# Optimization experiments

Measured on AMD Instinct MI355X. Metric: run time of the kernel, lower is better.

## Reference

```python
import jax, jax.numpy as jnp
import numpy as np

N_NODES = 50000
N_EDGES = 800000
NFEAT, NHID, NCLASS = 128, 256, 64


def setup_inputs() -> dict:
    key = jax.random.key(0)
    ks = jax.random.split(key, 8)
    x = jax.random.normal(ks[0], (N_NODES, NFEAT), dtype=jnp.float32)
    edge_index = jax.random.randint(ks[1], (2, N_EDGES), 0, N_NODES, dtype=jnp.int64)
    s1 = 1.0 / np.sqrt(NFEAT)
    s2 = 1.0 / np.sqrt(NHID)
    W1_neigh = jax.random.normal(ks[2], (NFEAT, NHID), dtype=jnp.float32) * s1
    W1_root = jax.random.normal(ks[3], (NFEAT, NHID), dtype=jnp.float32) * s1
    b1 = jnp.zeros((NHID,), dtype=jnp.float32)
    W2_neigh = jax.random.normal(ks[4], (NHID, NCLASS), dtype=jnp.float32) * s2
    W2_root = jax.random.normal(ks[5], (NHID, NCLASS), dtype=jnp.float32) * s2
    b2 = jnp.zeros((NCLASS,), dtype=jnp.float32)
    return {"x": x, "edge_index": edge_index, "W1_neigh": W1_neigh,
            "W1_root": W1_root, "b1": b1, "W2_neigh": W2_neigh,
            "W2_root": W2_root, "b2": b2}


def _sage_conv(h, src, dst, n_nodes, W_neigh, W_root, b):
    # mean aggregation of source features into destination nodes
    msg = h[src]                                                   # [E, d]
    summed = jax.ops.segment_sum(msg, dst, num_segments=n_nodes)   # [N, d]
    cnt = jax.ops.segment_sum(jnp.ones((src.shape[0],), h.dtype), dst,
                              num_segments=n_nodes)                # [N]
    mean = summed / jnp.maximum(cnt, 1.0)[:, None]
    return mean @ W_neigh + h @ W_root + b


def reference(x, edge_index, W1_neigh, W1_root, b1, W2_neigh, W2_root, b2):
    src, dst = edge_index[0], edge_index[1]
    n = x.shape[0]
    h = jax.nn.relu(_sage_conv(x, src, dst, n, W1_neigh, W1_root, b1))
    # dropout is identity in eval mode
    out = _sage_conv(h, src, dst, n, W2_neigh, W2_root, b2)
    return out
```

## Files before the change

### kernel.cpp

```cpp
#include <hip/hip_runtime.h>

#define N_NODES 50000
#define N_EDGES 800000
#define NFEAT   128
#define NHID    256
#define NCLASS  64

#define NPASS 8
#define PASS_W ((N_NODES + NPASS - 1) / NPASS)
#define ELLCAP 64

#define NPAIR   (N_EDGES / 2)
#define ECHUNK2 ((NPAIR + 255) / 256)
#define FILL_B  (ECHUNK2 * NPASS)
#define CVTX_B  ((N_NODES * 32 + 255) / 256)
#define CVTW_B  (((65536 + 32768) + 255) / 256)

typedef unsigned short u16;
typedef unsigned int   u32;
typedef __attribute__((ext_vector_type(8))) u16   u16x8;
typedef __attribute__((ext_vector_type(8))) short s16x8;
typedef __attribute__((ext_vector_type(4))) float f32x4;

__device__ inline u16 f2bf(float f) {
    u32 u = __float_as_uint(f);
    u32 r = (u + 0x7FFFu + ((u >> 16) & 1u)) >> 16;
    return (u16)r;
}
__device__ inline float bflo(u32 v) { return __uint_as_float(v << 16); }
__device__ inline float bfhi(u32 v) { return __uint_as_float(v & 0xFFFF0000u); }

#define GLOAD_LDS16(g, l)                                                        \
    __builtin_amdgcn_global_load_lds(                                            \
        (const __attribute__((address_space(1))) u32*)(const void*)(g),          \
        (__attribute__((address_space(3))) u32*)(void*)(l), 16, 0, 0)

__global__ __launch_bounds__(256) void prep_fill_kernel(const float* __restrict__ x,
                                                        const int* __restrict__ ei,
                                                        const float* __restrict__ W1r,
                                                        const float* __restrict__ W1n,
                                                        const float* __restrict__ W2n,
                                                        const float* __restrict__ W2r,
                                                        u16* __restrict__ xa,
                                                        int* __restrict__ cnt,
                                                        u16* __restrict__ ell,
                                                        u16* __restrict__ W1t,
                                                        u16* __restrict__ W2t) {
    int b = blockIdx.x;
    if (b < FILL_B) {
        int p = b & (NPASS - 1);
        int i = (b >> 3) * 256 + threadIdx.x;
        if (i >= NPAIR) return;
        int2 d2 = reinterpret_cast<const int2*>(ei + N_EDGES)[i];
        u32 lo = (u32)(p * PASS_W);
        bool in0 = ((u32)d2.x - lo) < (u32)PASS_W;
        bool in1 = ((u32)d2.y - lo) < (u32)PASS_W;
        if (in0 | in1) {
            int2 s2 = reinterpret_cast<const int2*>(ei)[i];
            if (in0) {
                int pos = atomicAdd(&cnt[d2.x], 1);
                if (pos < ELLCAP) ell[(size_t)d2.x * ELLCAP + pos] = (u16)s2.x;
            }
            if (in1) {
                int pos = atomicAdd(&cnt[d2.y], 1);
                if (pos < ELLCAP) ell[(size_t)d2.y * ELLCAP + pos] = (u16)s2.y;
            }
        }
    } else if (b < FILL_B + CVTX_B) {
        int idx = (b - FILL_B) * 256 + threadIdx.x;
        if (idx >= N_NODES * 32) return;
        int r  = idx >> 5;
        int c4 = (idx & 31) * 4;
        float4 v = *reinterpret_cast<const float4*>(x + (size_t)r * NFEAT + c4);
        uint2 o;
        o.x = (u32)f2bf(v.x) | ((u32)f2bf(v.y) << 16);
        o.y = (u32)f2bf(v.z) | ((u32)f2bf(v.w) << 16);
        *reinterpret_cast<uint2*>(xa + (size_t)r * 256 + c4) = o;
    } else {
        int id = (b - FILL_B - CVTX_B) * 256 + threadIdx.x;
        if (id < 65536) {
            int k = id & 255, n = id >> 8;
            float v = (k < NFEAT) ? W1r[(size_t)k * NHID + n]
                                  : W1n[(size_t)(k - NFEAT) * NHID + n];
            W1t[(size_t)n * 256 + k] = f2bf(v);
        } else if (id < 65536 + 32768) {
            int j = id - 65536;
            int k = j & 255, n = j >> 8;
            float v = (n < NCLASS) ? W2n[(size_t)k * NCLASS + n]
                                   : W2r[(size_t)k * NCLASS + (n - NCLASS)];
            W2t[(size_t)n * 256 + k] = f2bf(v);
        }
    }
}

__global__ __launch_bounds__(256) void gather1_kernel(const int* __restrict__ cnt,
                                                      const u16* __restrict__ ell,
                                                      u16* __restrict__ xa) {
    int gtid = blockIdx.x * 256 + threadIdx.x;
    int node = gtid >> 6;
    if (node >= N_NODES) return;
    int lane = threadIdx.x & 63;
    const u32* xrow = reinterpret_cast<const u32*>(xa);
    const u16* idx = ell + (size_t)node * ELLCAP;
    int deg = cnt[node];
    if (deg > ELLCAP) deg = ELLCAP;
    float ax = 0.0f, ay = 0.0f;
    int j = 0;
    for (; j + 16 <= deg; j += 16) {
        int s[16]; u32 v[16];
        #pragma unroll
        for (int q = 0; q < 16; ++q) s[q] = idx[j + q];
        #pragma unroll
        for (int q = 0; q < 16; ++q) v[q] = xrow[(size_t)s[q] * 128 + lane];
        #pragma unroll
        for (int q = 0; q < 16; ++q) { ax += bflo(v[q]); ay += bfhi(v[q]); }
    }
    for (; j + 8 <= deg; j += 8) {
        int s[8]; u32 v[8];
        #pragma unroll
        for (int q = 0; q < 8; ++q) s[q] = idx[j + q];
        #pragma unroll
        for (int q = 0; q < 8; ++q) v[q] = xrow[(size_t)s[q] * 128 + lane];
        #pragma unroll
        for (int q = 0; q < 8; ++q) { ax += bflo(v[q]); ay += bfhi(v[q]); }
    }
    for (; j < deg; ++j) {
        u32 v = xrow[(size_t)idx[j] * 128 + lane];
        ax += bflo(v);
        ay += bfhi(v);
    }
    float invd = 1.0f / fmaxf((float)deg, 1.0f);
    u32 packed = (u32)f2bf(ax * invd) | ((u32)f2bf(ay * invd) << 16);
    reinterpret_cast<u32*>(xa + (size_t)node * 256 + 128)[lane] = packed;
}

__global__ __launch_bounds__(256) void gather2_kernel(const int* __restrict__ cnt,
                                                      const u16* __restrict__ ell,
                                                      const u16* __restrict__ t,
                                                      float* __restrict__ out) {
    int gtid = blockIdx.x * 256 + threadIdx.x;
    int wave = gtid >> 6;
    int lane = threadIdx.x & 63;
    int node = wave * 2 + (lane >> 5);
    int l    = lane & 31;
    if (node >= N_NODES) return;
    const u32* trow = reinterpret_cast<const u32*>(t);
    const u16* idx = ell + (size_t)node * ELLCAP;
    int deg = cnt[node];
    if (deg > ELLCAP) deg = ELLCAP;
    float ax = 0.0f, ay = 0.0f;
    int j = 0;
    for (; j + 16 <= deg; j += 16) {
        int s[16]; u32 v[16];
        #pragma unroll
        for (int q = 0; q < 16; ++q) s[q] = idx[j + q];
        #pragma unroll
        for (int q = 0; q < 16; ++q) v[q] = trow[(size_t)s[q] * 32 + l];
        #pragma unroll
        for (int q = 0; q < 16; ++q) { ax += bflo(v[q]); ay += bfhi(v[q]); }
    }
    for (; j + 8 <= deg; j += 8) {
        int s[8]; u32 v[8];
        #pragma unroll
        for (int q = 0; q < 8; ++q) s[q] = idx[j + q];
        #pragma unroll
        for (int q = 0; q < 8; ++q) v[q] = trow[(size_t)s[q] * 32 + l];
        #pragma unroll
        for (int q = 0; q < 8; ++q) { ax += bflo(v[q]); ay += bfhi(v[q]); }
    }
    for (; j < deg; ++j) {
        u32 v = trow[(size_t)idx[j] * 32 + l];
        ax += bflo(v); ay += bfhi(v);
    }
    float invd = 1.0f / fmaxf((float)deg, 1.0f);
    float* o = out + (size_t)node * NCLASS + l * 2;
    o[0] += ax * invd;
    o[1] += ay * invd;
}

__global__ __launch_bounds__(256) void gemm1_mfma(const u16* __restrict__ xa,
                                                  const u16* __restrict__ W1t,
                                                  const float* __restrict__ b1,
                                                  u16* __restrict__ h) {
    __shared__ u16 As[128 * 32];
    __shared__ u16 Bs[128 * 32];
    const int tid = threadIdx.x;
    const int r0 = blockIdx.x * 128;
    const int n0 = blockIdx.y * 128;
    const int wid = tid >> 6, ln = tid & 63;
    const int wm = (wid & 1) * 64, wn = (wid >> 1) * 64;
    const int lr = ln & 15;
    const int lq = ln >> 4;

    f32x4 acc[4][4] = {};

    for (int k0 = 0; k0 < 256; k0 += 32) {
        #pragma unroll
        for (int it = 0; it < 2; ++it) {
            int c   = it * 256 + tid;
            int row = c >> 2;
            int ko  = (c & 3) * 8;
            GLOAD_LDS16(xa  + (size_t)(r0 + row) * 256 + k0 + ko, As + c * 8);
            GLOAD_LDS16(W1t + (size_t)(n0 + row) * 256 + k0 + ko, Bs + c * 8);
        }
        __syncthreads();

        s16x8 af[4], bf[4];
        #pragma unroll
        for (int i = 0; i < 4; ++i)
            af[i] = *reinterpret_cast<const s16x8*>(As + (wm + i * 16 + lr) * 32 + lq * 8);
        #pragma unroll
        for (int j = 0; j < 4; ++j)
            bf[j] = *reinterpret_cast<const s16x8*>(Bs + (wn + j * 16 + lr) * 32 + lq * 8);
        #pragma unroll
        for (int i = 0; i < 4; ++i)
            #pragma unroll
            for (int j = 0; j < 4; ++j)
                acc[i][j] = __builtin_amdgcn_mfma_f32_16x16x32_bf16(af[i], bf[j], acc[i][j], 0, 0, 0);
        __syncthreads();
    }

    #pragma unroll
    for (int i = 0; i < 4; ++i) {
        #pragma unroll
        for (int j = 0; j < 4; ++j) {
            int col = n0 + wn + j * 16 + lr;
            float bias = b1[col];
            #pragma unroll
            for (int r = 0; r < 4; ++r) {
                int row = r0 + wm + i * 16 + lq * 4 + r;
                if (row < N_NODES)
                    h[(size_t)row * 256 + col] = f2bf(fmaxf(acc[i][j][r] + bias, 0.0f));
            }
        }
    }
}

__global__ __launch_bounds__(256) void gemm2_mfma(const u16* __restrict__ h,
                                                  const u16* __restrict__ W2t,
                                                  const float* __restrict__ b2,
                                                  u16* __restrict__ t,
                                                  float* __restrict__ out) {
    __shared__ u16 As[128 * 32];
    __shared__ u16 Bs[128 * 32];
    const int tid = threadIdx.x;
    const int r0 = blockIdx.x * 128;
    const int wid = tid >> 6, ln = tid & 63;
    const int wm = (wid & 1) * 64, wn = (wid >> 1) * 64;
    const int lr = ln & 15;
    const int lq = ln >> 4;

    f32x4 acc[4][4] = {};

    for (int k0 = 0; k0 < 256; k0 += 32) {
        #pragma unroll
        for (int it = 0; it < 2; ++it) {
            int c   = it * 256 + tid;
            int row = c >> 2;
            int ko  = (c & 3) * 8;
            GLOAD_LDS16(h   + (size_t)(r0 + row) * 256 + k0 + ko, As + c * 8);
            GLOAD_LDS16(W2t + (size_t)row * 256 + k0 + ko,        Bs + c * 8);
        }
        __syncthreads();

        s16x8 af[4], bf[4];
        #pragma unroll
        for (int i = 0; i < 4; ++i)
            af[i] = *reinterpret_cast<const s16x8*>(As + (wm + i * 16 + lr) * 32 + lq * 8);
        #pragma unroll
        for (int j = 0; j < 4; ++j)
            bf[j] = *reinterpret_cast<const s16x8*>(Bs + (wn + j * 16 + lr) * 32 + lq * 8);
        #pragma unroll
        for (int i = 0; i < 4; ++i)
            #pragma unroll
            for (int j = 0; j < 4; ++j)
                acc[i][j] = __builtin_amdgcn_mfma_f32_16x16x32_bf16(af[i], bf[j], acc[i][j], 0, 0, 0);
        __syncthreads();
    }

    #pragma unroll
    for (int i = 0; i < 4; ++i) {
        #pragma unroll
        for (int j = 0; j < 4; ++j) {
            int col = wn + j * 16 + lr;
            #pragma unroll
            for (int r = 0; r < 4; ++r) {
                int row = r0 + wm + i * 16 + lq * 4 + r;
                if (row >= N_NODES) continue;
                if (col < NCLASS) {
                    t[(size_t)row * NCLASS + col] = f2bf(acc[i][j][r]);
                } else {
                    int c = col - NCLASS;
                    out[(size_t)row * NCLASS + c] = acc[i][j][r] + b2[c];
                }
            }
        }
    }
}

extern "C" void kernel_launch(void* const* d_in, const int* in_sizes, int n_in,
                              void* d_out, int out_size, void* d_ws, size_t ws_size,
                              hipStream_t stream) {
    const float* x    = (const float*)d_in[0];
    const int*   ei   = (const int*)d_in[1];
    const float* W1n  = (const float*)d_in[2];
    const float* W1r  = (const float*)d_in[3];
    const float* b1   = (const float*)d_in[4];
    const float* W2n  = (const float*)d_in[5];
    const float* W2r  = (const float*)d_in[6];
    const float* b2   = (const float*)d_in[7];
    float* out = (float*)d_out;

    int* cnt = (int*)d_ws;
    u16* ell = (u16*)(cnt + 50048);
    u16* xa  = ell + (size_t)N_NODES * ELLCAP;
    u16* h   = xa + (size_t)N_NODES * 256;
    u16* t   = h  + (size_t)N_NODES * 256;
    u16* W1t = t  + (size_t)N_NODES * 64;
    u16* W2t = W1t + 65536;

    hipMemsetAsync(cnt, 0, 50048 * sizeof(int), stream);

    prep_fill_kernel<<<FILL_B + CVTX_B + CVTW_B, 256, 0, stream>>>(
        x, ei, W1r, W1n, W2n, W2r, xa, cnt, ell, W1t, W2t);

    gather1_kernel<<<(N_NODES * 64 + 255) / 256, 256, 0, stream>>>(cnt, ell, xa);
    gemm1_mfma<<<dim3((N_NODES + 127) / 128, 2), 256, 0, stream>>>(xa, W1t, b1, h);

    gemm2_mfma<<<(N_NODES + 127) / 128, 256, 0, stream>>>(h, W2t, b2, t, out);
    gather2_kernel<<<(N_NODES * 32 + 255) / 256, 256, 0, stream>>>(cnt, ell, t, out);
}
```

Before: 227.4 us.

## Fuse all stages into one persistent cooperative kernel with grid syncs

```diff
diff --git a/kernel.cpp b/kernel.cpp
--- a/kernel.cpp
+++ b/kernel.cpp
@@ -1,4 +1,7 @@
 #include <hip/hip_runtime.h>
+#include <hip/hip_cooperative_groups.h>
+
+namespace cg = cooperative_groups;
 
 #define N_NODES 50000
 #define N_EDGES 800000
@@ -15,6 +18,9 @@
 #define FILL_B  (ECHUNK2 * NPASS)
 #define CVTX_B  ((N_NODES * 32 + 255) / 256)
 #define CVTW_B  (((65536 + 32768) + 255) / 256)
+
+#define G1_TILES 782
+#define G2_TILES 391
 
 typedef unsigned short u16;
 typedef unsigned int   u32;
@@ -35,265 +41,263 @@
         (const __attribute__((address_space(1))) u32*)(const void*)(g),          \
         (__attribute__((address_space(3))) u32*)(void*)(l), 16, 0, 0)
 
-__global__ __launch_bounds__(256) void prep_fill_kernel(const float* __restrict__ x,
-                                                        const int* __restrict__ ei,
-                                                        const float* __restrict__ W1r,
-                                                        const float* __restrict__ W1n,
-                                                        const float* __restrict__ W2n,
-                                                        const float* __restrict__ W2r,
-                                                        u16* __restrict__ xa,
-                                                        int* __restrict__ cnt,
-                                                        u16* __restrict__ ell,
-                                                        u16* __restrict__ W1t,
-                                                        u16* __restrict__ W2t) {
-    int b = blockIdx.x;
-    if (b < FILL_B) {
-        int p = b & (NPASS - 1);
-        int i = (b >> 3) * 256 + threadIdx.x;
-        if (i >= NPAIR) return;
-        int2 d2 = reinterpret_cast<const int2*>(ei + N_EDGES)[i];
-        u32 lo = (u32)(p * PASS_W);
-        bool in0 = ((u32)d2.x - lo) < (u32)PASS_W;
-        bool in1 = ((u32)d2.y - lo) < (u32)PASS_W;
-        if (in0 | in1) {
-            int2 s2 = reinterpret_cast<const int2*>(ei)[i];
-            if (in0) {
-                int pos = atomicAdd(&cnt[d2.x], 1);
-                if (pos < ELLCAP) ell[(size_t)d2.x * ELLCAP + pos] = (u16)s2.x;
-            }
-            if (in1) {
-                int pos = atomicAdd(&cnt[d2.y], 1);
-                if (pos < ELLCAP) ell[(size_t)d2.y * ELLCAP + pos] = (u16)s2.y;
-            }
-        }
-    } else if (b < FILL_B + CVTX_B) {
-        int idx = (b - FILL_B) * 256 + threadIdx.x;
-        if (idx >= N_NODES * 32) return;
-        int r  = idx >> 5;
-        int c4 = (idx & 31) * 4;
-        float4 v = *reinterpret_cast<const float4*>(x + (size_t)r * NFEAT + c4);
-        uint2 o;
-        o.x = (u32)f2bf(v.x) | ((u32)f2bf(v.y) << 16);
-        o.y = (u32)f2bf(v.z) | ((u32)f2bf(v.w) << 16);
-        *reinterpret_cast<uint2*>(xa + (size_t)r * 256 + c4) = o;
-    } else {
-        int id = (b - FILL_B - CVTX_B) * 256 + threadIdx.x;
-        if (id < 65536) {
-            int k = id & 255, n = id >> 8;
-            float v = (k < NFEAT) ? W1r[(size_t)k * NHID + n]
-                                  : W1n[(size_t)(k - NFEAT) * NHID + n];
-            W1t[(size_t)n * 256 + k] = f2bf(v);
-        } else if (id < 65536 + 32768) {
-            int j = id - 65536;
-            int k = j & 255, n = j >> 8;
-            float v = (n < NCLASS) ? W2n[(size_t)k * NCLASS + n]
-                                   : W2r[(size_t)k * NCLASS + (n - NCLASS)];
-            W2t[(size_t)n * 256 + k] = f2bf(v);
-        }
-    }
-}
-
-__global__ __launch_bounds__(256) void gather1_kernel(const int* __restrict__ cnt,
-                                                      const u16* __restrict__ ell,
-                                                      u16* __restrict__ xa) {
-    int gtid = blockIdx.x * 256 + threadIdx.x;
-    int node = gtid >> 6;
-    if (node >= N_NODES) return;
-    int lane = threadIdx.x & 63;
-    const u32* xrow = reinterpret_cast<const u32*>(xa);
-    const u16* idx = ell + (size_t)node * ELLCAP;
-    int deg = cnt[node];
-    if (deg > ELLCAP) deg = ELLCAP;
-    float ax = 0.0f, ay = 0.0f;
-    int j = 0;
-    for (; j + 16 <= deg; j += 16) {
-        int s[16]; u32 v[16];
-        #pragma unroll
-        for (int q = 0; q < 16; ++q) s[q] = idx[j + q];
-        #pragma unroll
-        for (int q = 0; q < 16; ++q) v[q] = xrow[(size_t)s[q] * 128 + lane];
-        #pragma unroll
-        for (int q = 0; q < 16; ++q) { ax += bflo(v[q]); ay += bfhi(v[q]); }
-    }
-    for (; j + 8 <= deg; j += 8) {
-        int s[8]; u32 v[8];
-        #pragma unroll
-        for (int q = 0; q < 8; ++q) s[q] = idx[j + q];
-        #pragma unroll
-        for (int q = 0; q < 8; ++q) v[q] = xrow[(size_t)s[q] * 128 + lane];
-        #pragma unroll
-        for (int q = 0; q < 8; ++q) { ax += bflo(v[q]); ay += bfhi(v[q]); }
-    }
-    for (; j < deg; ++j) {
-        u32 v = xrow[(size_t)idx[j] * 128 + lane];
-        ax += bflo(v);
-        ay += bfhi(v);
-    }
-    float invd = 1.0f / fmaxf((float)deg, 1.0f);
-    u32 packed = (u32)f2bf(ax * invd) | ((u32)f2bf(ay * invd) << 16);
-    reinterpret_cast<u32*>(xa + (size_t)node * 256 + 128)[lane] = packed;
-}
-
-__global__ __launch_bounds__(256) void gather2_kernel(const int* __restrict__ cnt,
-                                                      const u16* __restrict__ ell,
-                                                      const u16* __restrict__ t,
-                                                      float* __restrict__ out) {
-    int gtid = blockIdx.x * 256 + threadIdx.x;
-    int wave = gtid >> 6;
-    int lane = threadIdx.x & 63;
-    int node = wave * 2 + (lane >> 5);
-    int l    = lane & 31;
-    if (node >= N_NODES) return;
-    const u32* trow = reinterpret_cast<const u32*>(t);
-    const u16* idx = ell + (size_t)node * ELLCAP;
-    int deg = cnt[node];
-    if (deg > ELLCAP) deg = ELLCAP;
-    float ax = 0.0f, ay = 0.0f;
-    int j = 0;
-    for (; j + 16 <= deg; j += 16) {
-        int s[16]; u32 v[16];
-        #pragma unroll
-        for (int q = 0; q < 16; ++q) s[q] = idx[j + q];
-        #pragma unroll
-        for (int q = 0; q < 16; ++q) v[q] = trow[(size_t)s[q] * 32 + l];
-        #pragma unroll
-        for (int q = 0; q < 16; ++q) { ax += bflo(v[q]); ay += bfhi(v[q]); }
-    }
-    for (; j + 8 <= deg; j += 8) {
-        int s[8]; u32 v[8];
-        #pragma unroll
-        for (int q = 0; q < 8; ++q) s[q] = idx[j + q];
-        #pragma unroll
-        for (int q = 0; q < 8; ++q) v[q] = trow[(size_t)s[q] * 32 + l];
-        #pragma unroll
-        for (int q = 0; q < 8; ++q) { ax += bflo(v[q]); ay += bfhi(v[q]); }
-    }
-    for (; j < deg; ++j) {
-        u32 v = trow[(size_t)idx[j] * 32 + l];
-        ax += bflo(v); ay += bfhi(v);
-    }
-    float invd = 1.0f / fmaxf((float)deg, 1.0f);
-    float* o = out + (size_t)node * NCLASS + l * 2;
-    o[0] += ax * invd;
-    o[1] += ay * invd;
-}
-
-__global__ __launch_bounds__(256) void gemm1_mfma(const u16* __restrict__ xa,
-                                                  const u16* __restrict__ W1t,
-                                                  const float* __restrict__ b1,
-                                                  u16* __restrict__ h) {
+__global__ __launch_bounds__(256) void uber_kernel(
+    const float* __restrict__ x,   const int* __restrict__ ei,
+    const float* __restrict__ W1r, const float* __restrict__ W1n,
+    const float* __restrict__ W2n, const float* __restrict__ W2r,
+    const float* __restrict__ b1,  const float* __restrict__ b2,
+    int* __restrict__ cnt, u16* __restrict__ ell,
+    u16* __restrict__ xa,  u16* __restrict__ h, u16* __restrict__ t,
+    u16* __restrict__ W1t, u16* __restrict__ W2t,
+    float* __restrict__ out)
+{
+    cg::grid_group grid = cg::this_grid();
+    const int tid = threadIdx.x;
+    const int nb  = gridDim.x;
+
     __shared__ u16 As[128 * 32];
     __shared__ u16 Bs[128 * 32];
-    const int tid = threadIdx.x;
-    const int r0 = blockIdx.x * 128;
-    const int n0 = blockIdx.y * 128;
-    const int wid = tid >> 6, ln = tid & 63;
-    const int wm = (wid & 1) * 64, wn = (wid >> 1) * 64;
-    const int lr = ln & 15;
-    const int lq = ln >> 4;
-
-    f32x4 acc[4][4] = {};
-
-    for (int k0 = 0; k0 < 256; k0 += 32) {
-        #pragma unroll
-        for (int it = 0; it < 2; ++it) {
-            int c   = it * 256 + tid;
-            int row = c >> 2;
-            int ko  = (c & 3) * 8;
-            GLOAD_LDS16(xa  + (size_t)(r0 + row) * 256 + k0 + ko, As + c * 8);
-            GLOAD_LDS16(W1t + (size_t)(n0 + row) * 256 + k0 + ko, Bs + c * 8);
-        }
-        __syncthreads();
-
-        s16x8 af[4], bf[4];
-        #pragma unroll
-        for (int i = 0; i < 4; ++i)
-            af[i] = *reinterpret_cast<const s16x8*>(As + (wm + i * 16 + lr) * 32 + lq * 8);
-        #pragma unroll
-        for (int j = 0; j < 4; ++j)
-            bf[j] = *reinterpret_cast<const s16x8*>(Bs + (wn + j * 16 + lr) * 32 + lq * 8);
-        #pragma unroll
-        for (int i = 0; i < 4; ++i)
+
+    for (int i = blockIdx.x * 256 + tid; i < 50048; i += nb * 256) cnt[i] = 0;
+    grid.sync();
+
+    for (int b = blockIdx.x; b < FILL_B + CVTX_B + CVTW_B; b += nb) {
+        if (b < FILL_B) {
+            int p = b & (NPASS - 1);
+            int i = (b >> 3) * 256 + tid;
+            if (i < NPAIR) {
+                int2 d2 = reinterpret_cast<const int2*>(ei + N_EDGES)[i];
+                u32 lo = (u32)(p * PASS_W);
+                bool in0 = ((u32)d2.x - lo) < (u32)PASS_W;
+                bool in1 = ((u32)d2.y - lo) < (u32)PASS_W;
+                if (in0 | in1) {
+                    int2 s2 = reinterpret_cast<const int2*>(ei)[i];
+                    if (in0) {
+                        int pos = atomicAdd(&cnt[d2.x], 1);
+                        if (pos < ELLCAP) ell[(size_t)d2.x * ELLCAP + pos] = (u16)s2.x;
+                    }
+                    if (in1) {
+                        int pos = atomicAdd(&cnt[d2.y], 1);
+                        if (pos < ELLCAP) ell[(size_t)d2.y * ELLCAP + pos] = (u16)s2.y;
+                    }
+                }
+            }
+        } else if (b < FILL_B + CVTX_B) {
+            int idx = (b - FILL_B) * 256 + tid;
+            if (idx < N_NODES * 32) {
+                int r  = idx >> 5;
+                int c4 = (idx & 31) * 4;
+                float4 v = *reinterpret_cast<const float4*>(x + (size_t)r * NFEAT + c4);
+                uint2 o;
+                o.x = (u32)f2bf(v.x) | ((u32)f2bf(v.y) << 16);
+                o.y = (u32)f2bf(v.z) | ((u32)f2bf(v.w) << 16);
+                *reinterpret_cast<uint2*>(xa + (size_t)r * 256 + c4) = o;
+            }
+        } else {
+            int id = (b - FILL_B - CVTX_B) * 256 + tid;
+            if (id < 65536) {
+                int k = id & 255, n = id >> 8;
+                float v = (k < NFEAT) ? W1r[(size_t)k * NHID + n]
+                                      : W1n[(size_t)(k - NFEAT) * NHID + n];
+                W1t[(size_t)n * 256 + k] = f2bf(v);
+            } else if (id < 65536 + 32768) {
+                int j = id - 65536;
+                int k = j & 255, n = j >> 8;
+                float v = (n < NCLASS) ? W2n[(size_t)k * NCLASS + n]
+                                       : W2r[(size_t)k * NCLASS + (n - NCLASS)];
+                W2t[(size_t)n * 256 + k] = f2bf(v);
+            }
+        }
+    }
+    grid.sync();
+
+    {
+        const u32* xrow = reinterpret_cast<const u32*>(xa);
+        int lane   = tid & 63;
+        int gwave  = (blockIdx.x * 256 + tid) >> 6;
+        int nwaves = (nb * 256) >> 6;
+        for (int node = gwave; node < N_NODES; node += nwaves) {
+            const u16* idx = ell + (size_t)node * ELLCAP;
+            int deg = cnt[node];
+            if (deg > ELLCAP) deg = ELLCAP;
+            float ax = 0.0f, ay = 0.0f;
+            int j = 0;
+            for (; j + 16 <= deg; j += 16) {
+                int s[16]; u32 v[16];
+                #pragma unroll
+                for (int q = 0; q < 16; ++q) s[q] = idx[j + q];
+                #pragma unroll
+                for (int q = 0; q < 16; ++q) v[q] = xrow[(size_t)s[q] * 128 + lane];
+                #pragma unroll
+                for (int q = 0; q < 16; ++q) { ax += bflo(v[q]); ay += bfhi(v[q]); }
+            }
+            for (; j + 8 <= deg; j += 8) {
+                int s[8]; u32 v[8];
+                #pragma unroll
+                for (int q = 0; q < 8; ++q) s[q] = idx[j + q];
+                #pragma unroll
+                for (int q = 0; q < 8; ++q) v[q] = xrow[(size_t)s[q] * 128 + lane];
+                #pragma unroll
+                for (int q = 0; q < 8; ++q) { ax += bflo(v[q]); ay += bfhi(v[q]); }
+            }
+            for (; j < deg; ++j) {
+                u32 v = xrow[(size_t)idx[j] * 128 + lane];
+                ax += bflo(v);
+                ay += bfhi(v);
+            }
+            float invd = 1.0f / fmaxf((float)deg, 1.0f);
+            u32 packed = (u32)f2bf(ax * invd) | ((u32)f2bf(ay * invd) << 16);
+            reinterpret_cast<u32*>(xa + (size_t)node * 256 + 128)[lane] = packed;
+        }
+    }
+    grid.sync();
+
+    {
+        const int wid = tid >> 6, ln = tid & 63;
+        const int wm = (wid & 1) * 64, wn = (wid >> 1) * 64;
+        const int lr = ln & 15;
+        const int lq = ln >> 4;
+        for (int vb = blockIdx.x; vb < G1_TILES; vb += nb) {
+            int by = (vb >= 391) ? 1 : 0;
+            int bx = vb - 391 * by;
+            int r0 = bx * 128, n0 = by * 128;
+
+            f32x4 acc[4][4] = {};
+            for (int k0 = 0; k0 < 256; k0 += 32) {
+                #pragma unroll
+                for (int it = 0; it < 2; ++it) {
+                    int c   = it * 256 + tid;
+                    int row = c >> 2;
+                    int ko  = (c & 3) * 8;
+                    GLOAD_LDS16(xa  + (size_t)(r0 + row) * 256 + k0 + ko, As + c * 8);
+                    GLOAD_LDS16(W1t + (size_t)(n0 + row) * 256 + k0 + ko, Bs + c * 8);
+                }
+                __syncthreads();
+                s16x8 af[4], bf[4];
+                #pragma unroll
+                for (int i = 0; i < 4; ++i)
+                    af[i] = *reinterpret_cast<const s16x8*>(As + (wm + i * 16 + lr) * 32 + lq * 8);
+                #pragma unroll
+                for (int j = 0; j < 4; ++j)
+                    bf[j] = *reinterpret_cast<const s16x8*>(Bs + (wn + j * 16 + lr) * 32 + lq * 8);
+                #pragma unroll
+                for (int i = 0; i < 4; ++i)
+                    #pragma unroll
+                    for (int j = 0; j < 4; ++j)
+                        acc[i][j] = __builtin_amdgcn_mfma_f32_16x16x32_bf16(af[i], bf[j], acc[i][j], 0, 0, 0);
+                __syncthreads();
+            }
             #pragma unroll
-            for (int j = 0; j < 4; ++j)
-                acc[i][j] = __builtin_amdgcn_mfma_f32_16x16x32_bf16(af[i], bf[j], acc[i][j], 0, 0, 0);
-        __syncthreads();
-    }
-
-    #pragma unroll
-    for (int i = 0; i < 4; ++i) {
-        #pragma unroll
-        for (int j = 0; j < 4; ++j) {
-            int col = n0 + wn + j * 16 + lr;
-            float bias = b1[col];
+            for (int i = 0; i < 4; ++i) {
+                #pragma unroll
+                for (int j = 0; j < 4; ++j) {
+                    int col = n0 + wn + j * 16 + lr;
+                    float bias = b1[col];
+                    #pragma unroll
+                    for (int r = 0; r < 4; ++r) {
+                        int row = r0 + wm + i * 16 + lq * 4 + r;
+                        if (row < N_NODES)
+                            h[(size_t)row * 256 + col] = f2bf(fmaxf(acc[i][j][r] + bias, 0.0f));
+                    }
+                }
+            }
+        }
+    }
+    grid.sync();
+
+    {
+        const int wid = tid >> 6, ln = tid & 63;
+        const int wm = (wid & 1) * 64, wn = (wid >> 1) * 64;
+        const int lr = ln & 15;
+        const int lq = ln >> 4;
+        for (int vb = blockIdx.x; vb < G2_TILES; vb += nb) {
+            int r0 = vb * 128;
+            f32x4 acc[4][4] = {};
+            for (int k0 = 0; k0 < 256; k0 += 32) {
+                #pragma unroll
+                for (int it = 0; it < 2; ++it) {
+                    int c   = it * 256 + tid;
+                    int row = c >> 2;
+                    int ko  = (c & 3) * 8;
+                    GLOAD_LDS16(h   + (size_t)(r0 + row) * 256 + k0 + ko, As + c * 8);
+                    GLOAD_LDS16(W2t + (size_t)row * 256 + k0 + ko,        Bs + c * 8);
+                }
+                __syncthreads();
+                s16x8 af[4], bf[4];
+                #pragma unroll
+                for (int i = 0; i < 4; ++i)
+                    af[i] = *reinterpret_cast<const s16x8*>(As + (wm + i * 16 + lr) * 32 + lq * 8);
+                #pragma unroll
+                for (int j = 0; j < 4; ++j)
+                    bf[j] = *reinterpret_cast<const s16x8*>(Bs + (wn + j * 16 + lr) * 32 + lq * 8);
+                #pragma unroll
+                for (int i = 0; i < 4; ++i)
+                    #pragma unroll
+                    for (int j = 0; j < 4; ++j)
+                        acc[i][j] = __builtin_amdgcn_mfma_f32_16x16x32_bf16(af[i], bf[j], acc[i][j], 0, 0, 0);
+                __syncthreads();
+            }
             #pragma unroll
-            for (int r = 0; r < 4; ++r) {
-                int row = r0 + wm + i * 16 + lq * 4 + r;
-                if (row < N_NODES)
-                    h[(size_t)row * 256 + col] = f2bf(fmaxf(acc[i][j][r] + bias, 0.0f));
-            }
-        }
-    }
-}
-
-__global__ __launch_bounds__(256) void gemm2_mfma(const u16* __restrict__ h,
-                                                  const u16* __restrict__ W2t,
-                                                  const float* __restrict__ b2,
-                                                  u16* __restrict__ t,
-                                                  float* __restrict__ out) {
-    __shared__ u16 As[128 * 32];
-    __shared__ u16 Bs[128 * 32];
-    const int tid = threadIdx.x;
-    const int r0 = blockIdx.x * 128;
-    const int wid = tid >> 6, ln = tid & 63;
-    const int wm = (wid & 1) * 64, wn = (wid >> 1) * 64;
-    const int lr = ln & 15;
-    const int lq = ln >> 4;
-
-    f32x4 acc[4][4] = {};
-
-    for (int k0 = 0; k0 < 256; k0 += 32) {
-        #pragma unroll
-        for (int it = 0; it < 2; ++it) {
-            int c   = it * 256 + tid;
-            int row = c >> 2;
-            int ko  = (c & 3) * 8;
-            GLOAD_LDS16(h   + (size_t)(r0 + row) * 256 + k0 + ko, As + c * 8);
-            GLOAD_LDS16(W2t + (size_t)row * 256 + k0 + ko,        Bs + c * 8);
-        }
-        __syncthreads();
-
-        s16x8 af[4], bf[4];
-        #pragma unroll
-        for (int i = 0; i < 4; ++i)
-            af[i] = *reinterpret_cast<const s16x8*>(As + (wm + i * 16 + lr) * 32 + lq * 8);
-        #pragma unroll
-        for (int j = 0; j < 4; ++j)
-            bf[j] = *reinterpret_cast<const s16x8*>(Bs + (wn + j * 16 + lr) * 32 + lq * 8);
-        #pragma unroll
-        for (int i = 0; i < 4; ++i)
-            #pragma unroll
-            for (int j = 0; j < 4; ++j)
-                acc[i][j] = __builtin_amdgcn_mfma_f32_16x16x32_bf16(af[i], bf[j], acc[i][j], 0, 0, 0);
-        __syncthreads();
-    }
-
-    #pragma unroll
-    for (int i = 0; i < 4; ++i) {
-        #pragma unroll
-        for (int j = 0; j < 4; ++j) {
-            int col = wn + j * 16 + lr;
-            #pragma unroll
-            for (int r = 0; r < 4; ++r) {
-                int row = r0 + wm + i * 16 + lq * 4 + r;
-                if (row >= N_NODES) continue;
-                if (col < NCLASS) {
-                    t[(size_t)row * NCLASS + col] = f2bf(acc[i][j][r]);
-                } else {
-                    int c = col - NCLASS;
-                    out[(size_t)row * NCLASS + c] = acc[i][j][r] + b2[c];
-                }
-            }
+            for (int i = 0; i < 4; ++i) {
+                #pragma unroll
+                for (int j = 0; j < 4; ++j) {
+                    int col = wn + j * 16 + lr;
+                    #pragma unroll
+                    for (int r = 0; r < 4; ++r) {
+                        int row = r0 + wm + i * 16 + lq * 4 + r;
+                        if (row >= N_NODES) continue;
+                        if (col < NCLASS) {
+                            t[(size_t)row * NCLASS + col] = f2bf(acc[i][j][r]);
+                        } else {
+                            int c = col - NCLASS;
+                            out[(size_t)row * NCLASS + c] = acc[i][j][r] + b2[c];
+                        }
+                    }
+                }
+            }
+        }
+    }
+    grid.sync();
+
+    {
+        const u32* trow = reinterpret_cast<const u32*>(t);
+        int lane   = tid & 63;
+        int gwave  = (blockIdx.x * 256 + tid) >> 6;
+        int nwaves = (nb * 256) >> 6;
+        int l    = lane & 31;
+        for (int w = gwave; w < N_NODES / 2; w += nwaves) {
+            int node = w * 2 + (lane >> 5);
+            const u16* idx = ell + (size_t)node * ELLCAP;
+            int deg = cnt[node];
+            if (deg > ELLCAP) deg = ELLCAP;
+            float ax = 0.0f, ay = 0.0f;
+            int j = 0;
+            for (; j + 16 <= deg; j += 16) {
+                int s[16]; u32 v[16];
+                #pragma unroll
+                for (int q = 0; q < 16; ++q) s[q] = idx[j + q];
+                #pragma unroll
+                for (int q = 0; q < 16; ++q) v[q] = trow[(size_t)s[q] * 32 + l];
+                #pragma unroll
+                for (int q = 0; q < 16; ++q) { ax += bflo(v[q]); ay += bfhi(v[q]); }
+            }
+            for (; j + 8 <= deg; j += 8) {
+                int s[8]; u32 v[8];
+                #pragma unroll
+                for (int q = 0; q < 8; ++q) s[q] = idx[j + q];
+                #pragma unroll
+                for (int q = 0; q < 8; ++q) v[q] = trow[(size_t)s[q] * 32 + l];
+                #pragma unroll
+                for (int q = 0; q < 8; ++q) { ax += bflo(v[q]); ay += bfhi(v[q]); }
+            }
+            for (; j < deg; ++j) {
+                u32 v = trow[(size_t)idx[j] * 32 + l];
+                ax += bflo(v); ay += bfhi(v);
+            }
+            float invd = 1.0f / fmaxf((float)deg, 1.0f);
+            float* o = out + (size_t)node * NCLASS + l * 2;
+            o[0] += ax * invd;
+            o[1] += ay * invd;
         }
     }
 }
@@ -319,14 +323,16 @@
     u16* W1t = t  + (size_t)N_NODES * 64;
     u16* W2t = W1t + 65536;
 
-    hipMemsetAsync(cnt, 0, 50048 * sizeof(int), stream);
-
-    prep_fill_kernel<<<FILL_B + CVTX_B + CVTW_B, 256, 0, stream>>>(
-        x, ei, W1r, W1n, W2n, W2r, xa, cnt, ell, W1t, W2t);
-
-    gather1_kernel<<<(N_NODES * 64 + 255) / 256, 256, 0, stream>>>(cnt, ell, xa);
-    gemm1_mfma<<<dim3((N_NODES + 127) / 128, 2), 256, 0, stream>>>(xa, W1t, b1, h);
-
-    gemm2_mfma<<<(N_NODES + 127) / 128, 256, 0, stream>>>(h, W2t, b2, t, out);
-    gather2_kernel<<<(N_NODES * 32 + 255) / 256, 256, 0, stream>>>(cnt, ell, t, out);
+    int occ = 0;
+    hipOccupancyMaxActiveBlocksPerMultiprocessor(&occ, uber_kernel, 256, 0);
+    if (occ < 1) occ = 1;
+    if (occ > 8) occ = 8;
+    unsigned grid = (unsigned)occ * 256u;
+
+    void* args[] = { (void*)&x, (void*)&ei, (void*)&W1r, (void*)&W1n,
+                     (void*)&W2n, (void*)&W2r, (void*)&b1, (void*)&b2,
+                     (void*)&cnt, (void*)&ell, (void*)&xa, (void*)&h,
+                     (void*)&t, (void*)&W1t, (void*)&W2t, (void*)&out };
+    hipLaunchCooperativeKernel((const void*)uber_kernel, dim3(grid), dim3(256),
+                               args, 0, stream);
 }
```

Result: slower. 600.4 us (+164.0%).
